# Optimization experiments

Measured on AMD Instinct MI355X. Metric: run time of the kernel, lower is better.

Reference implementation:

```python
import jax, jax.numpy as jnp
import numpy as np

B, N, NFEAT, NHID, NHEADS, NBLK = 8, 512, 32, 128, 4, 6


def _lrelu(x):
    return jax.nn.leaky_relu(x, 0.01)


def _layernorm(x, eps=1e-5):
    m = jnp.mean(x, axis=-1, keepdims=True)
    v = jnp.mean((x - m) ** 2, axis=-1, keepdims=True)
    return (x - m) / jnp.sqrt(v + eps)


def _gat(x, W, a, mask, concat):
    # x:[b,n,f]  W:[H,f,o]  a:[H,2o]  mask:[b,n,n] bool
    o = W.shape[-1]
    Wh = jnp.einsum('bnf,hfo->hbno', x, W)
    s1 = jnp.einsum('hbno,ho->hbn', Wh, a[:, :o])   # Wh @ a[:o]
    s2 = jnp.einsum('hbno,ho->hbn', Wh, a[:, o:])   # Wh @ a[o:]
    # rank-1 score: e[i,j] = leakyrelu(s1[i]*s2[j])
    e = _lrelu(s1[:, :, :, None] * s2[:, :, None, :])  # [h,b,n,n]
    e = jnp.where(mask[None], e, jnp.float32(-9e15))
    att = jax.nn.softmax(e, axis=-1)
    att = jnp.where(mask[None], att, jnp.float32(0.0))
    hp = jnp.einsum('hbij,hbjo->hbio', att, Wh)
    return jax.nn.elu(hp) if concat else hp


def _attn_block(x, W, a, rW, rb, mask):
    res = x
    h = _gat(x, W, a, mask, True)                      # [H,b,n,o]
    h = jnp.moveaxis(h, 0, 2).reshape(x.shape[0], x.shape[1], -1)  # concat heads
    h = h @ rW + rb
    if h.shape[-1] == res.shape[-1]:
        h = h + res
    return _layernorm(h)


def _fel(x, f1w1, f1b1, f1w2, f1b2, f2w1, f2b1, f2w2, f2b2, f3w1, f3b1, f3w2, f3b2):
    res = _lrelu(_lrelu(x @ f1w1 + f1b1) @ f1w2 + f1b2)
    h = _lrelu(_lrelu(res @ f2w1 + f2b1) @ f2w2 + f2b2)
    x = _layernorm(h + res)
    res = x
    h = _lrelu(res @ f3w1 + f3b1) @ f3w2 + f3b2
    return _layernorm(h + res)


def setup_inputs() -> dict:
    key = jax.random.key(0)
    ks = iter(jax.random.split(key, 24))
    nrm = lambda shape: jax.random.normal(next(ks), shape, jnp.float32) * 0.05
    inp = {}
    inp['x'] = jax.random.normal(next(ks), (B, N, NFEAT), jnp.float32)
    inp['adj'] = jax.random.randint(next(ks), (B, N, N), 0, 2, jnp.int32)
    inp['layer_id'] = 0
    inp['f1w1'] = nrm((NFEAT, NHID)); inp['f1b1'] = jnp.zeros((NHID,), jnp.float32)
    inp['f1w2'] = nrm((NHID, NHID)); inp['f1b2'] = jnp.zeros((NHID,), jnp.float32)
    inp['f2w1'] = nrm((NHID, 2 * NHID)); inp['f2b1'] = jnp.zeros((2 * NHID,), jnp.float32)
    inp['f2w2'] = nrm((2 * NHID, NHID)); inp['f2b2'] = jnp.zeros((NHID,), jnp.float32)
    inp['f3w1'] = nrm((NHID, 2 * NHID)); inp['f3b1'] = jnp.zeros((2 * NHID,), jnp.float32)
    inp['f3w2'] = nrm((2 * NHID, NHID)); inp['f3b2'] = jnp.zeros((NHID,), jnp.float32)
    inp['att_W'] = nrm((NBLK, NHEADS, NHID, NHID))
    inp['att_a'] = nrm((NBLK, NHEADS, 2 * NHID))
    inp['resh_W'] = nrm((NBLK, NHEADS * NHID, NHID))
    inp['resh_b'] = jnp.zeros((NBLK, NHID), jnp.float32)
    inp['out_W'] = nrm((2, NHID, NHID))
    inp['out_a'] = nrm((2, 2 * NHID))
    inp['proj_W'] = nrm((2 * NHID, 1))
    inp['proj_b'] = jnp.zeros((1,), jnp.float32)
    return inp


def reference(x, adj, layer_id, f1w1, f1b1, f1w2, f1b2, f2w1, f2b1, f2w2, f2b2,
              f3w1, f3b1, f3w2, f3b2, att_W, att_a, resh_W, resh_b, out_W, out_a,
              proj_W, proj_b):
    mask = adj > 0
    mask_t = jnp.transpose(adj, (0, 2, 1)) > 0
    h = _fel(x, f1w1, f1b1, f1w2, f1b2, f2w1, f2b1, f2w2, f2b2, f3w1, f3b1, f3w2, f3b2)
    for i in range(3):
        h = _attn_block(h, att_W[i], att_a[i], resh_W[i], resh_b[i], mask)
    h = _lrelu(_gat(h, out_W[0:1], out_a[0:1], mask, False)[0])
    ht = h
    for i in range(3, 6):
        ht = _attn_block(ht, att_W[i], att_a[i], resh_W[i], resh_b[i], mask_t)
    ht = _lrelu(_gat(ht, out_W[1:2], out_a[1:2], mask_t, False)[0])
    z = jnp.concatenate([h, ht], axis=-1)   # [b,n,2*nhid]
    z = jnp.mean(z, axis=1)                 # sum/length
    return jnp.squeeze(z @ proj_W + proj_b, axis=1)
```

## Files before the change

kernel.cpp:

```cpp
#include <hip/hip_runtime.h>
#include <math.h>

#define B 8
#define N 512
#define D 128
#define H 4
#define TOK (B*N)

typedef __attribute__((ext_vector_type(8))) short bfrag;
typedef __attribute__((ext_vector_type(4))) float facc;
typedef unsigned short u16;
typedef unsigned int u32;
typedef unsigned long long u64;

__device__ __forceinline__ float lrelu(float x){ return x > 0.f ? x : 0.01f*x; }
__device__ __forceinline__ u16 f2bf(float f){
  u32 u = __float_as_uint(f);
  u += 0x7fffu + ((u >> 16) & 1u);
  return (u16)(u >> 16);
}
__device__ __forceinline__ u32 pk2(float a, float b){
  return (u32)f2bf(a) | ((u32)f2bf(b) << 16);
}

#define LS 72

__global__ void prep_kernel(const int* __restrict__ adj,
    u32* __restrict__ mbits, u32* __restrict__ mtbits,
    const float* s0, const float* s1_, const float* s2_, const float* s3,
    const float* s4, const float* s5, const float* s6, const float* s7,
    const float* s8,
    u16* d0, u16* d1, u16* d2, u16* d3, u16* d4, u16* d5, u16* d6, u16* d7, u16* d8)
{
  __shared__ int smem[64*65];
  const int tid = threadIdx.x;
  if (blockIdx.x < 512){
    const int tb = blockIdx.x;
    const int b = tb >> 6, i0 = ((tb >> 3) & 7)*64, j0 = (tb & 7)*64;
    #pragma unroll
    for (int i = 0; i < 4; ++i){
      const int r = i*16 + (tid >> 4);
      const int c = (tid & 15)*4;
      int4 v = *(const int4*)&adj[((size_t)b*N + i0 + r)*N + j0 + c];
      smem[r*65 + c]     = v.x; smem[r*65 + c + 1] = v.y;
      smem[r*65 + c + 2] = v.z; smem[r*65 + c + 3] = v.w;
    }
    __syncthreads();
    const int wv = tid >> 6, lane = tid & 63;
    #pragma unroll
    for (int q = 0; q < 16; ++q){
      const int r = wv*16 + q;
      u64 bf_ = __ballot(smem[r*65 + lane] > 0);
      if (lane == 0)
        *(u64*)&mbits[((size_t)b*N + i0 + r)*16 + (j0 >> 5)] = bf_;
      u64 bt_ = __ballot(smem[lane*65 + r] > 0);
      if (lane == 0)
        *(u64*)&mtbits[((size_t)b*N + j0 + r)*16 + (i0 >> 5)] = bt_;
    }
  } else {
    float* ftile = (float*)smem;
    const int tx = tid & 31, ty = tid >> 5;
    const float* srcs[9] = {s0,s1_,s2_,s3,s4,s5,s6,s7,s8};
    u16* dsts[9] = {d0,d1,d2,d3,d4,d5,d6,d7,d8};
    const int Ks[9] = {32,128,128,256,128,256,128,128,512};
    const int Ns[9] = {128,128,256,128,256,128,128,128,128};
    const int zs[9] = {1,1,1,1,1,1,24,2,6};
    const int job = (int)blockIdx.x - 512;
    int m = 0, base = 0;
    for (; m < 9; ++m){
      int cnt = (Ks[m]>>5)*(Ns[m]>>5)*zs[m];
      if (job < base + cnt) break;
      base += cnt;
    }
    const int rem = job - base;
    const int tn = Ns[m] >> 5;
    const int per = (Ks[m] >> 5)*tn;
    const int z = rem / per, t = rem % per;
    const int k0 = (t / tn)*32, n0 = (t % tn)*32;
    const float* src = srcs[m] + (size_t)z*Ks[m]*Ns[m];
    u16* dst = dsts[m] + (size_t)z*Ks[m]*Ns[m];
    for (int r = ty; r < 32; r += 8)
      ftile[r*33 + tx] = src[(size_t)(k0+r)*Ns[m] + n0 + tx];
    __syncthreads();
    for (int r = ty; r < 32; r += 8)
      dst[(size_t)(n0+r)*Ks[m] + k0 + tx] = f2bf(ftile[tx*33 + r]);
  }
}

__device__ __forceinline__ void stageB64(const u16* __restrict__ BTn, int ldb,
                                         int k0, u16* Bs, int tid){
  const int n = tid >> 1, part = tid & 1;
  const u16* wp = BTn + (size_t)n*ldb + k0 + part*32;
  uint4 w0 = *(const uint4*)wp,      w1 = *(const uint4*)(wp+8);
  uint4 w2 = *(const uint4*)(wp+16), w3 = *(const uint4*)(wp+24);
  *(uint4*)&Bs[n*LS + part*32]      = w0;
  *(uint4*)&Bs[n*LS + part*32 + 8]  = w1;
  *(uint4*)&Bs[n*LS + part*32 + 16] = w2;
  *(uint4*)&Bs[n*LS + part*32 + 24] = w3;
}
__device__ __forceinline__ void stageB32(const u16* __restrict__ BTn, int ldb,
                                         int k0, u16* Bs, int tid){
  const int n = tid >> 1, part = tid & 1;
  const u16* wp = BTn + (size_t)n*ldb + k0 + part*16;
  uint4 w0 = *(const uint4*)wp, w1 = *(const uint4*)(wp+8);
  *(uint4*)&Bs[n*LS + part*16]     = w0;
  *(uint4*)&Bs[n*LS + part*16 + 8] = w1;
}

__device__ __forceinline__ void mfma64(const u16* As, const u16* Bs,
                                       facc acc[4], int r0, int c0,
                                       int quad, int l15){
  #pragma unroll
  for (int kk = 0; kk < 2; ++kk){
    bfrag af = *(const bfrag*)&As[(r0 + l15)*LS + kk*32 + quad*8];
    #pragma unroll
    for (int g = 0; g < 4; ++g){
      bfrag bf = *(const bfrag*)&Bs[(c0 + g*16 + l15)*LS + kk*32 + quad*8];
      acc[g] = __builtin_amdgcn_mfma_f32_16x16x32_bf16(af, bf, acc[g], 0,0,0);
    }
  }
}
__device__ __forceinline__ void mfma32(const u16* As, const u16* Bs,
                                       facc acc[4], int r0, int c0,
                                       int quad, int l15){
  bfrag af = *(const bfrag*)&As[(r0 + l15)*LS + quad*8];
  #pragma unroll
  for (int g = 0; g < 4; ++g){
    bfrag bf = *(const bfrag*)&Bs[(c0 + g*16 + l15)*LS + quad*8];
    acc[g] = __builtin_amdgcn_mfma_f32_16x16x32_bf16(af, bf, acc[g], 0,0,0);
  }
}

__device__ __forceinline__ void mfma64w(const u16* As, const u16* Bs,
                                        facc acc[2][2], int c0,
                                        int quad, int l15){
  #pragma unroll
  for (int kk = 0; kk < 2; ++kk){
    bfrag af0 = *(const bfrag*)&As[(l15)*LS      + kk*32 + quad*8];
    bfrag af1 = *(const bfrag*)&As[(16 + l15)*LS + kk*32 + quad*8];
    #pragma unroll
    for (int f = 0; f < 2; ++f){
      bfrag bf = *(const bfrag*)&Bs[(c0 + f*16 + l15)*LS + kk*32 + quad*8];
      acc[0][f] = __builtin_amdgcn_mfma_f32_16x16x32_bf16(af0, bf, acc[0][f], 0,0,0);
      acc[1][f] = __builtin_amdgcn_mfma_f32_16x16x32_bf16(af1, bf, acc[1][f], 0,0,0);
    }
  }
}

template<int ACT, int FIN>
__global__ __launch_bounds__(256) void gemm32(
    const float* __restrict__ A, int lda, int K,
    const u16* __restrict__ BT, const float* __restrict__ bias,
    const float* __restrict__ res, float* __restrict__ out, int ldo)
{
  const int tid = threadIdx.x;
  const int t0 = blockIdx.x * 32;
  const int n0 = blockIdx.y * 128;
  __shared__ __align__(16) u16 As[2][32*LS];
  __shared__ __align__(16) u16 Bs[2][128*LS];
  __shared__ float scrS[4][16], scrQ[4][16];
  const int wave = tid >> 6, lane = tid & 63, quad = lane >> 4, l15 = lane & 15;
  const int r0 = (wave & 1)*16, c0 = (wave >> 1)*64;
  facc acc[4];
  #pragma unroll
  for (int g = 0; g < 4; ++g) acc[g] = (facc){0.f,0.f,0.f,0.f};
  const u16* BTn = BT + (size_t)n0*K;

  const int arow = tid >> 3, ako = tid & 7;
  const float* aptr = A + (size_t)(t0+arow)*lda;
  const int bn = tid >> 1, bpart = tid & 1;
  const u16* bptr = BTn + (size_t)bn*K;

  const int nt = K >> 6;
  int kfin = 0;
  if (nt > 0){
    { const float* ap = aptr + ako*8;
      float4 a0 = *(const float4*)ap, a1 = *(const float4*)(ap+4);
      uint4 u = { pk2(a0.x,a0.y), pk2(a0.z,a0.w), pk2(a1.x,a1.y), pk2(a1.z,a1.w) };
      *(uint4*)&As[0][arow*LS + ako*8] = u;
      const u16* wp = bptr + bpart*32;
      uint4 g0 = *(const uint4*)wp,      g1 = *(const uint4*)(wp+8);
      uint4 g2 = *(const uint4*)(wp+16), g3 = *(const uint4*)(wp+24);
      u16* bp = &Bs[0][bn*LS + bpart*32];
      *(uint4*)bp = g0; *(uint4*)(bp+8) = g1; *(uint4*)(bp+16) = g2; *(uint4*)(bp+24) = g3;
    }
    __syncthreads();
    for (int k = 0; k < nt - 1; ++k){
      const int cur = k & 1, nxt = cur ^ 1;
      const float* ap = aptr + (k+1)*64 + ako*8;
      float4 a0 = *(const float4*)ap, a1 = *(const float4*)(ap+4);
      const u16* wp = bptr + (k+1)*64 + bpart*32;
      uint4 n0v = *(const uint4*)wp,      n1v = *(const uint4*)(wp+8);
      uint4 n2v = *(const uint4*)(wp+16), n3v = *(const uint4*)(wp+24);
      mfma64(As[cur], Bs[cur], acc, r0, c0, quad, l15);
      { uint4 u = { pk2(a0.x,a0.y), pk2(a0.z,a0.w), pk2(a1.x,a1.y), pk2(a1.z,a1.w) };
        *(uint4*)&As[nxt][arow*LS + ako*8] = u;
        u16* bp = &Bs[nxt][bn*LS + bpart*32];
        *(uint4*)bp = n0v; *(uint4*)(bp+8) = n1v; *(uint4*)(bp+16) = n2v; *(uint4*)(bp+24) = n3v; }
      __syncthreads();
    }
    kfin = (nt-1) & 1;
    mfma64(As[kfin], Bs[kfin], acc, r0, c0, quad, l15);
  }
  if (K & 63){
    if (nt > 0) __syncthreads();
    const int k0 = nt*64;
    { float4 a0 = *(const float4*)(aptr + k0 + ako*4);
      uint2 u = { pk2(a0.x,a0.y), pk2(a0.z,a0.w) };
      *(uint2*)&As[kfin][arow*LS + ako*4] = u;
    }
    stageB32(BTn, K, k0, Bs[kfin], tid);
    __syncthreads();
    mfma32(As[kfin], Bs[kfin], acc, r0, c0, quad, l15);
  }

  float bv[4];
  #pragma unroll
  for (int g = 0; g < 4; ++g) bv[g] = bias[n0 + c0 + g*16 + l15];

  if (FIN == 0){
    #pragma unroll
    for (int g = 0; g < 4; ++g){
      const int c = n0 + c0 + g*16 + l15;
      #pragma unroll
      for (int q = 0; q < 4; ++q){
        const int rq = t0 + r0 + quad*4 + q;
        float xv = acc[g][q] + bv[g];
        if (ACT) xv = lrelu(xv);
        out[(size_t)rq*ldo + c] = xv;
      }
    }
  } else {
    float v[4][4], s[4] = {0,0,0,0}, sq[4] = {0,0,0,0};
    #pragma unroll
    for (int g = 0; g < 4; ++g){
      const int c = c0 + g*16 + l15;
      #pragma unroll
      for (int q = 0; q < 4; ++q){
        const int rq = t0 + r0 + quad*4 + q;
        float xv = acc[g][q] + bv[g];
        if (ACT) xv = lrelu(xv);
        xv += res[(size_t)rq*128 + c];
        v[g][q] = xv; s[q] += xv; sq[q] += xv*xv;
      }
    }
    #pragma unroll
    for (int m = 1; m < 16; m <<= 1){
      #pragma unroll
      for (int q = 0; q < 4; ++q){ s[q] += __shfl_xor(s[q], m, 64); sq[q] += __shfl_xor(sq[q], m, 64); }
    }
    __syncthreads();
    if (l15 == 0){
      #pragma unroll
      for (int q = 0; q < 4; ++q){ scrS[wave][quad*4+q] = s[q]; scrQ[wave][quad*4+q] = sq[q]; }
    }
    __syncthreads();
    #pragma unroll
    for (int q = 0; q < 4; ++q){
      const int rq = t0 + r0 + quad*4 + q;
      const float fs = s[q] + scrS[wave^2][quad*4+q];
      const float fq = sq[q] + scrQ[wave^2][quad*4+q];
      const float mean = fs*(1.f/D);
      const float rstd = rsqrtf(fq*(1.f/D) - mean*mean + 1e-5f);
      #pragma unroll
      for (int g = 0; g < 4; ++g)
        out[(size_t)rq*128 + c0 + g*16 + l15] = (v[g][q] - mean)*rstd;
    }
  }
}

__global__ __launch_bounds__(256) void gemm32b(
    const u16* __restrict__ A, int lda, int K,
    const u16* __restrict__ BT, const float* __restrict__ bias,
    const float* __restrict__ res, float* __restrict__ out)
{
  const int tid = threadIdx.x;
  const int t0 = blockIdx.x * 32;
  __shared__ __align__(16) u16 As[2][32*LS];
  __shared__ __align__(16) u16 Bs[2][128*LS];
  __shared__ float scrS[4][32], scrQ[4][32];
  const int wave = tid >> 6, lane = tid & 63, quad = lane >> 4, l15 = lane & 15;
  const int c0 = wave*32;
  facc acc[2][2];
  #pragma unroll
  for (int rg = 0; rg < 2; ++rg)
    #pragma unroll
    for (int f = 0; f < 2; ++f) acc[rg][f] = (facc){0.f,0.f,0.f,0.f};

  const int arow = tid >> 3, ako = tid & 7;
  const u16* aptr = A + (size_t)(t0+arow)*lda + ako*8;
  const int bn = tid >> 1, bpart = tid & 1;
  const u16* bptr = BT + (size_t)bn*K + bpart*32;

  { uint4 ga = *(const uint4*)aptr;
    uint4 g0 = *(const uint4*)bptr,      g1 = *(const uint4*)(bptr+8);
    uint4 g2 = *(const uint4*)(bptr+16), g3 = *(const uint4*)(bptr+24);
    *(uint4*)&As[0][arow*LS + ako*8] = ga;
    u16* bp = &Bs[0][bn*LS + bpart*32];
    *(uint4*)bp = g0; *(uint4*)(bp+8) = g1; *(uint4*)(bp+16) = g2; *(uint4*)(bp+24) = g3;
  }
  __syncthreads();

  const int nt = K >> 6;
  for (int k = 0; k < nt - 1; ++k){
    const int cur = k & 1, nxt = cur ^ 1;
    uint4 na = *(const uint4*)(aptr + (k+1)*64);
    const u16* wp = bptr + (k+1)*64;
    uint4 n0 = *(const uint4*)wp,      n1 = *(const uint4*)(wp+8);
    uint4 n2 = *(const uint4*)(wp+16), n3 = *(const uint4*)(wp+24);
    mfma64w(As[cur], Bs[cur], acc, c0, quad, l15);
    *(uint4*)&As[nxt][arow*LS + ako*8] = na;
    { u16* bp = &Bs[nxt][bn*LS + bpart*32];
      *(uint4*)bp = n0; *(uint4*)(bp+8) = n1; *(uint4*)(bp+16) = n2; *(uint4*)(bp+24) = n3; }
    __syncthreads();
  }
  mfma64w(As[(nt-1)&1], Bs[(nt-1)&1], acc, c0, quad, l15);

  float bv[2];
  #pragma unroll
  for (int f = 0; f < 2; ++f) bv[f] = bias[c0 + f*16 + l15];
  float v[2][2][4], s[2][4], sq[2][4];
  #pragma unroll
  for (int rg = 0; rg < 2; ++rg)
    #pragma unroll
    for (int q = 0; q < 4; ++q){ s[rg][q] = 0.f; sq[rg][q] = 0.f; }
  #pragma unroll
  for (int rg = 0; rg < 2; ++rg){
    #pragma unroll
    for (int f = 0; f < 2; ++f){
      const int c = c0 + f*16 + l15;
      #pragma unroll
      for (int q = 0; q < 4; ++q){
        const int rq = t0 + rg*16 + quad*4 + q;
        float xv = acc[rg][f][q] + bv[f] + res[(size_t)rq*128 + c];
        v[rg][f][q] = xv; s[rg][q] += xv; sq[rg][q] += xv*xv;
      }
    }
  }
  #pragma unroll
  for (int m = 1; m < 16; m <<= 1){
    #pragma unroll
    for (int rg = 0; rg < 2; ++rg)
      #pragma unroll
      for (int q = 0; q < 4; ++q){ s[rg][q] += __shfl_xor(s[rg][q], m, 64); sq[rg][q] += __shfl_xor(sq[rg][q], m, 64); }
  }
  if (l15 == 0){
    #pragma unroll
    for (int rg = 0; rg < 2; ++rg)
      #pragma unroll
      for (int q = 0; q < 4; ++q){
        scrS[wave][rg*16 + quad*4 + q] = s[rg][q];
        scrQ[wave][rg*16 + quad*4 + q] = sq[rg][q];
      }
  }
  __syncthreads();
  #pragma unroll
  for (int rg = 0; rg < 2; ++rg){
    #pragma unroll
    for (int q = 0; q < 4; ++q){
      const int row = rg*16 + quad*4 + q;
      const float fs = scrS[0][row] + scrS[1][row] + scrS[2][row] + scrS[3][row];
      const float fq = scrQ[0][row] + scrQ[1][row] + scrQ[2][row] + scrQ[3][row];
      const float mean = fs*(1.f/D);
      const float rstd = rsqrtf(fq*(1.f/D) - mean*mean + 1e-5f);
      #pragma unroll
      for (int f = 0; f < 2; ++f)
        out[(size_t)(t0+row)*128 + c0 + f*16 + l15] = (v[rg][f][q] - mean)*rstd;
    }
  }
}

__global__ __launch_bounds__(256) void wh32(
    const float* __restrict__ hin, const u16* __restrict__ WT,
    const float* __restrict__ a, u16* __restrict__ WhT,
    float* __restrict__ s1, float* __restrict__ s2)
{
  const int tid = threadIdx.x;
  const int h  = blockIdx.x >> 7;
  const int t0 = (blockIdx.x & 127) * 32;
  const int b = t0 >> 9, j0 = t0 & (N-1);
  __shared__ __align__(16) u16 As[2][32*LS];
  __shared__ __align__(16) u16 Bs[2][128*LS];
  __shared__ float r1s[2][32], r2s[2][32];
  const int wave = tid >> 6, lane = tid & 63, quad = lane >> 4, l15 = lane & 15;
  const int r0 = (wave & 1)*16, c0 = (wave >> 1)*64;
  facc acc[4];
  #pragma unroll
  for (int g = 0; g < 4; ++g) acc[g] = (facc){0.f,0.f,0.f,0.f};

  const int arow = tid >> 3, ako = tid & 7;
  const float* aptr = hin + (size_t)(t0+arow)*D + ako*8;
  const int bn = tid >> 1, bpart = tid & 1;
  const u16* bwp = WT + (size_t)h*D*D + (size_t)bn*D + bpart*32;

  { float4 a0 = *(const float4*)aptr, a1 = *(const float4*)(aptr+4);
    uint4 u = { pk2(a0.x,a0.y), pk2(a0.z,a0.w), pk2(a1.x,a1.y), pk2(a1.z,a1.w) };
    *(uint4*)&As[0][arow*LS + ako*8] = u;
    uint4 g0 = *(const uint4*)bwp,      g1 = *(const uint4*)(bwp+8);
    uint4 g2 = *(const uint4*)(bwp+16), g3 = *(const uint4*)(bwp+24);
    u16* bp = &Bs[0][bn*LS + bpart*32];
    *(uint4*)bp = g0; *(uint4*)(bp+8) = g1; *(uint4*)(bp+16) = g2; *(uint4*)(bp+24) = g3;
  }
  __syncthreads();
  { float4 a0 = *(const float4*)(aptr+64), a1 = *(const float4*)(aptr+68);
    uint4 g0 = *(const uint4*)(bwp+64),    g1 = *(const uint4*)(bwp+72);
    uint4 g2 = *(const uint4*)(bwp+80),    g3 = *(const uint4*)(bwp+88);
    mfma64(As[0], Bs[0], acc, r0, c0, quad, l15);
    uint4 u = { pk2(a0.x,a0.y), pk2(a0.z,a0.w), pk2(a1.x,a1.y), pk2(a1.z,a1.w) };
    *(uint4*)&As[1][arow*LS + ako*8] = u;
    u16* bp = &Bs[1][bn*LS + bpart*32];
    *(uint4*)bp = g0; *(uint4*)(bp+8) = g1; *(uint4*)(bp+16) = g2; *(uint4*)(bp+24) = g3;
  }
  __syncthreads();
  mfma64(As[1], Bs[1], acc, r0, c0, quad, l15);

  const float* ah = a + (size_t)h*2*D;
  const size_t obase = (size_t)(h*8 + b)*128;
  float p1[4] = {0,0,0,0}, p2[4] = {0,0,0,0};
  #pragma unroll
  for (int g = 0; g < 4; ++g){
    const int c = c0 + g*16 + l15;
    const float a1v = ah[c], a2v = ah[D + c];
    ushort4 wv;
    wv.x = f2bf(acc[g][0]); wv.y = f2bf(acc[g][1]);
    wv.z = f2bf(acc[g][2]); wv.w = f2bf(acc[g][3]);
    *(ushort4*)&WhT[(obase + c)*N + j0 + r0 + quad*4] = wv;
    #pragma unroll
    for (int q = 0; q < 4; ++q){
      p1[q] = fmaf(acc[g][q], a1v, p1[q]);
      p2[q] = fmaf(acc[g][q], a2v, p2[q]);
    }
  }
  #pragma unroll
  for (int m = 1; m < 16; m <<= 1){
    #pragma unroll
    for (int q = 0; q < 4; ++q){ p1[q] += __shfl_xor(p1[q], m, 64); p2[q] += __shfl_xor(p2[q], m, 64); }
  }
  if (l15 == 0){
    #pragma unroll
    for (int q = 0; q < 4; ++q){
      r1s[wave>>1][r0 + quad*4 + q] = p1[q];
      r2s[wave>>1][r0 + quad*4 + q] = p2[q];
    }
  }
  __syncthreads();
  if (tid < 32){
    s1[(size_t)h*TOK + t0 + tid] = r1s[0][tid] + r1s[1][tid];
    s2[(size_t)h*TOK + t0 + tid] = r2s[0][tid] + r2s[1][tid];
  }
}

__device__ __forceinline__ float score8(const float* s2s, const unsigned char* mrow,
                                        float s1lr, int k0, int lq, u16* asp){
  float4 sa = *(const float4*)&s2s[k0 + lq*8];
  float4 sb = *(const float4*)&s2s[k0 + lq*8 + 4];
  const u32 mm = mrow[(k0 >> 3) + lq];
  float ss[8] = {sa.x,sa.y,sa.z,sa.w,sb.x,sb.y,sb.z,sb.w};
  float v[8]; float p = 0.f;
  #pragma unroll
  for (int i = 0; i < 8; ++i){
    float e = lrelu(s1lr * ss[i]);
    float ex = ((mm >> i) & 1u) ? __expf(e) : 0.f;
    v[i] = ex; p += ex;
  }
  uint4 u = { pk2(v[0],v[1]), pk2(v[2],v[3]), pk2(v[4],v[5]), pk2(v[6],v[7]) };
  *(uint4*)asp = u;
  return p;
}

template<int MODE, int OBF>
__global__ __launch_bounds__(256) void pv32(
    const float* __restrict__ s1, const float* __restrict__ s2,
    const u32* __restrict__ mbits, const u16* __restrict__ WhT,
    void* __restrict__ out_, int ldo, int hcs)
{
  const int tid = threadIdx.x;
  const int h  = blockIdx.x >> 7;
  const int t0 = (blockIdx.x & 127) * 32;
  const int b = t0 >> 9, i0 = t0 & (N-1);
  __shared__ float s2s[N];
  __shared__ float s1s[32], sums[32];
  __shared__ u32 mbs[32*16];
  __shared__ __align__(16) u16 As[2][32*LS];
  __shared__ __align__(16) u16 Bs[2][128*LS];

  s2s[tid]     = s2[(size_t)h*TOK + b*N + tid];
  s2s[tid+256] = s2[(size_t)h*TOK + b*N + tid + 256];
  if (tid < 32) s1s[tid] = s1[(size_t)h*TOK + t0 + tid];
  { const int r = tid >> 3, wd = (tid & 7)*2;
    *(uint2*)&mbs[r*16 + wd] = *(const uint2*)&mbits[((size_t)b*N + i0 + r)*16 + wd];
  }

  const u16* BTn = WhT + (size_t)(h*8 + b)*128*N;
  const int wave = tid >> 6, lane = tid & 63, quad = lane >> 4, l15 = lane & 15;
  const int c0 = wave*32;
  facc acc[2][2];
  #pragma unroll
  for (int rg = 0; rg < 2; ++rg)
    #pragma unroll
    for (int f = 0; f < 2; ++f) acc[rg][f] = (facc){0.f,0.f,0.f,0.f};

  const int lr = tid >> 3, lq = tid & 7;
  const unsigned char* mrow = (const unsigned char*)&mbs[lr*16];
  const int bn = tid >> 1, bpart = tid & 1;
  const u16* bwp = BTn + (size_t)bn*N + bpart*32;
  float psum = 0.f;

  uint4 g0 = *(const uint4*)bwp,      g1 = *(const uint4*)(bwp+8);
  uint4 g2 = *(const uint4*)(bwp+16), g3 = *(const uint4*)(bwp+24);
  __syncthreads();
  const float s1lr = s1s[lr];
  psum += score8(s2s, mrow, s1lr, 0, lq, &As[0][lr*LS + lq*8]);
  { u16* bp = &Bs[0][bn*LS + bpart*32];
    *(uint4*)bp = g0; *(uint4*)(bp+8) = g1; *(uint4*)(bp+16) = g2; *(uint4*)(bp+24) = g3; }
  __syncthreads();

  #pragma unroll
  for (int k = 0; k < 7; ++k){
    const int cur = k & 1, nxt = cur ^ 1;
    const u16* wp = bwp + (k+1)*64;
    uint4 n0 = *(const uint4*)wp,      n1 = *(const uint4*)(wp+8);
    uint4 n2 = *(const uint4*)(wp+16), n3 = *(const uint4*)(wp+24);
    psum += score8(s2s, mrow, s1lr, (k+1)*64, lq, &As[nxt][lr*LS + lq*8]);
    mfma64w(As[cur], Bs[cur], acc, c0, quad, l15);
    { u16* bp = &Bs[nxt][bn*LS + bpart*32];
      *(uint4*)bp = n0; *(uint4*)(bp+8) = n1; *(uint4*)(bp+16) = n2; *(uint4*)(bp+24) = n3; }
    __syncthreads();
  }
  mfma64w(As[1], Bs[1], acc, c0, quad, l15);

  #pragma unroll
  for (int m = 1; m < 8; m <<= 1) psum += __shfl_xor(psum, m, 64);
  if (lq == 0) sums[lr] = psum;
  __syncthreads();

  #pragma unroll
  for (int rg = 0; rg < 2; ++rg){
    #pragma unroll
    for (int q = 0; q < 4; ++q){
      const int row = rg*16 + quad*4 + q;
      const float sv = sums[row];
      const float inv = sv > 0.f ? 1.f/sv : 0.f;
      const int rq = t0 + row;
      #pragma unroll
      for (int f = 0; f < 2; ++f){
        float xv = acc[rg][f][q] * inv;
        xv = (MODE == 0) ? (xv > 0.f ? xv : __expf(xv) - 1.f) : lrelu(xv);
        const size_t idx = (size_t)rq*ldo + h*hcs + c0 + f*16 + l15;
        if (OBF) ((u16*)out_)[idx] = f2bf(xv);
        else     ((float*)out_)[idx] = xv;
      }
    }
  }
}

__global__ void final_kernel(const float* __restrict__ hF, const float* __restrict__ hT,
                             const float* __restrict__ pW, const float* __restrict__ pb,
                             float* __restrict__ out)
{
  const int b = blockIdx.x, c = threadIdx.x;
  __shared__ float scr[4];
  const float* src = (c < D) ? (hF + (size_t)b*N*D + c) : (hT + (size_t)b*N*D + (c - D));
  float s = 0.f;
  for (int n = 0; n < N; ++n) s += src[(size_t)n*D];
  s *= (1.f/N);
  float p = s * pW[c];
  #pragma unroll
  for (int m = 32; m; m >>= 1) p += __shfl_xor(p, m, 64);
  __syncthreads();
  if ((c & 63) == 0) scr[c >> 6] = p;
  __syncthreads();
  if (c == 0) out[b] = scr[0] + scr[1] + scr[2] + scr[3] + pb[0];
}

extern "C" void kernel_launch(void* const* d_in, const int* in_sizes, int n_in,
                              void* d_out, int out_size, void* d_ws, size_t ws_size,
                              hipStream_t stream)
{
  (void)in_sizes; (void)n_in; (void)out_size; (void)ws_size;
  const float* x    = (const float*)d_in[0];
  const int*   adj  = (const int*)d_in[1];
  const float* f1w1 = (const float*)d_in[3];
  const float* f1b1 = (const float*)d_in[4];
  const float* f1w2 = (const float*)d_in[5];
  const float* f1b2 = (const float*)d_in[6];
  const float* f2w1 = (const float*)d_in[7];
  const float* f2b1 = (const float*)d_in[8];
  const float* f2w2 = (const float*)d_in[9];
  const float* f2b2 = (const float*)d_in[10];
  const float* f3w1 = (const float*)d_in[11];
  const float* f3b1 = (const float*)d_in[12];
  const float* f3w2 = (const float*)d_in[13];
  const float* f3b2 = (const float*)d_in[14];
  const float* attW = (const float*)d_in[15];
  const float* attA = (const float*)d_in[16];
  const float* rshW = (const float*)d_in[17];
  const float* rshB = (const float*)d_in[18];
  const float* outW = (const float*)d_in[19];
  const float* outA = (const float*)d_in[20];
  const float* pW   = (const float*)d_in[21];
  const float* pb   = (const float*)d_in[22];

  char* w = (char*)d_ws;
  float* hA  = (float*)w; w += (size_t)TOK*128*4;
  float* hB  = (float*)w; w += (size_t)TOK*128*4;
  float* hF  = (float*)w; w += (size_t)TOK*128*4;
  float* hq  = (float*)w; w += (size_t)TOK*256*4;
  u16*  hp2  = (u16*)w;  w += (size_t)TOK*512*2;
  u16*  WhT  = (u16*)w;  w += (size_t)H*8*128*N*2;
  float* s1  = (float*)w; w += (size_t)H*TOK*4;
  float* s2  = (float*)w; w += (size_t)H*TOK*4;
  u32* mbits = (u32*)w;  w += (size_t)B*N*16*4;
  u32* mtbits= (u32*)w;  w += (size_t)B*N*16*4;
  u16* f1w1T = (u16*)w; w += 128*32*2;
  u16* f1w2T = (u16*)w; w += 128*128*2;
  u16* f2w1T = (u16*)w; w += 256*128*2;
  u16* f2w2T = (u16*)w; w += 128*256*2;
  u16* f3w1T = (u16*)w; w += 256*128*2;
  u16* f3w2T = (u16*)w; w += 128*256*2;
  u16* attWT = (u16*)w; w += (size_t)24*128*128*2;
  u16* outWT = (u16*)w; w += (size_t)2*128*128*2;
  u16* rshWT = (u16*)w; w += (size_t)6*128*512*2;

  prep_kernel<<<1460,256,0,stream>>>(adj, mbits, mtbits,
      f1w1, f1w2, f2w1, f2w2, f3w1, f3w2, attW, outW, rshW,
      f1w1T, f1w2T, f2w1T, f2w2T, f3w1T, f3w2T, attWT, outWT, rshWT);

  gemm32<1,0><<<dim3(128,1),256,0,stream>>>(x,   32, 32,  f1w1T, f1b1, nullptr, hF, 128);
  gemm32<1,0><<<dim3(128,1),256,0,stream>>>(hF, 128, 128, f1w2T, f1b2, nullptr, hB, 128);
  gemm32<1,0><<<dim3(128,2),256,0,stream>>>(hB, 128, 128, f2w1T, f2b1, nullptr, hq, 256);
  gemm32<1,1><<<dim3(128,1),256,0,stream>>>(hq, 256, 256, f2w2T, f2b2, hB, hF, 128);
  gemm32<1,0><<<dim3(128,2),256,0,stream>>>(hF, 128, 128, f3w1T, f3b1, nullptr, hq, 256);
  gemm32<0,1><<<dim3(128,1),256,0,stream>>>(hq, 256, 256, f3w2T, f3b2, hF, hA, 128);

  float* cur = hA; float* nxt = hB;
  for (int i = 0; i < 3; ++i){
    wh32<<<H*128,256,0,stream>>>(cur, attWT + (size_t)i*H*D*D,
                                 attA + (size_t)i*H*2*D, WhT, s1, s2);
    pv32<0,1><<<H*128,256,0,stream>>>(s1, s2, mbits, WhT, hp2, 512, 128);
    gemm32b<<<128,256,0,stream>>>(hp2, 512, 512,
        rshWT + (size_t)i*128*512, rshB + (size_t)i*D, cur, nxt);
    float* t_ = cur; cur = nxt; nxt = t_;
  }
  wh32<<<128,256,0,stream>>>(cur, outWT, outA, WhT, s1, s2);
  pv32<1,0><<<128,256,0,stream>>>(s1, s2, mbits, WhT, hF, 128, 0);

  cur = hF; nxt = hA;
  for (int i = 3; i < 6; ++i){
    wh32<<<H*128,256,0,stream>>>(cur, attWT + (size_t)i*H*D*D,
                                 attA + (size_t)i*H*2*D, WhT, s1, s2);
    pv32<0,1><<<H*128,256,0,stream>>>(s1, s2, mtbits, WhT, hp2, 512, 128);
    gemm32b<<<128,256,0,stream>>>(hp2, 512, 512,
        rshWT + (size_t)i*128*512, rshB + (size_t)i*D, cur, nxt);
    cur = nxt; nxt = (cur == hA) ? hB : hA;
  }
  wh32<<<128,256,0,stream>>>(cur, outWT + 128*128, outA + 2*D, WhT, s1, s2);
  pv32<1,0><<<128,256,0,stream>>>(s1, s2, mtbits, WhT, nxt, 128, 0);

  final_kernel<<<B,2*D,0,stream>>>(hF, nxt, pW, pb, (float*)d_out);
}
```

Baseline: 333.9 us.

## Fuse FEL MLP chain, reshape+Wh projection, and output GAT with next-block projection

Replaces the six separate FEL GEMM launches with one kernel that keeps every intermediate in shared memory as bf16 and then computes the first attention block's Wh projection and scores. The reshape GEMM is fused with the next block's Wh/score projection, and the output GAT kernel also computes the transposed branch's first projection, accumulating column sums with atomics so the final mean no longer rereads full activations. This cuts the launch count from about 27 to 16 and removes global round trips for intermediates. In exchange it adds register and shared-memory pressure, and fewer blocks (128) now carry the Wh work that previously ran on 512.

```diff
diff --git a/kernel.cpp b/kernel.cpp
--- a/kernel.cpp
+++ b/kernel.cpp
@@ -24,9 +24,12 @@
 }
 
 #define LS 72
+#define ASF 264
+#define ASW 136
 
 __global__ void prep_kernel(const int* __restrict__ adj,
     u32* __restrict__ mbits, u32* __restrict__ mtbits,
+    float* __restrict__ colsumF, float* __restrict__ colsumT,
     const float* s0, const float* s1_, const float* s2_, const float* s3,
     const float* s4, const float* s5, const float* s6, const float* s7,
     const float* s8,
@@ -57,7 +60,7 @@
       if (lane == 0)
         *(u64*)&mtbits[((size_t)b*N + j0 + r)*16 + (i0 >> 5)] = bt_;
     }
-  } else {
+  } else if (blockIdx.x < 1460){
     float* ftile = (float*)smem;
     const int tx = tid & 31, ty = tid >> 5;
     const float* srcs[9] = {s0,s1_,s2_,s3,s4,s5,s6,s7,s8};
@@ -84,19 +87,26 @@
     __syncthreads();
     for (int r = ty; r < 32; r += 8)
       dst[(size_t)(n0+r)*Ks[m] + k0 + tx] = f2bf(ftile[tx*33 + r]);
-  }
-}
-
-__device__ __forceinline__ void stageB64(const u16* __restrict__ BTn, int ldb,
-                                         int k0, u16* Bs, int tid){
+  } else {
+    float4 z = {0.f,0.f,0.f,0.f};
+    *(float4*)&colsumF[tid*4] = z;
+    *(float4*)&colsumT[tid*4] = z;
+  }
+}
+
+struct BPre { uint4 a,b,c,d; };
+__device__ __forceinline__ BPre preB64(const u16* __restrict__ BTn, int ldb, int k0, int tid){
   const int n = tid >> 1, part = tid & 1;
   const u16* wp = BTn + (size_t)n*ldb + k0 + part*32;
-  uint4 w0 = *(const uint4*)wp,      w1 = *(const uint4*)(wp+8);
-  uint4 w2 = *(const uint4*)(wp+16), w3 = *(const uint4*)(wp+24);
-  *(uint4*)&Bs[n*LS + part*32]      = w0;
-  *(uint4*)&Bs[n*LS + part*32 + 8]  = w1;
-  *(uint4*)&Bs[n*LS + part*32 + 16] = w2;
-  *(uint4*)&Bs[n*LS + part*32 + 24] = w3;
+  BPre r;
+  r.a = *(const uint4*)wp;      r.b = *(const uint4*)(wp+8);
+  r.c = *(const uint4*)(wp+16); r.d = *(const uint4*)(wp+24);
+  return r;
+}
+__device__ __forceinline__ void landB64(const BPre& p, u16* Bs, int tid){
+  const int n = tid >> 1, part = tid & 1;
+  u16* bp = &Bs[n*LS + part*32];
+  *(uint4*)bp = p.a; *(uint4*)(bp+8) = p.b; *(uint4*)(bp+16) = p.c; *(uint4*)(bp+24) = p.d;
 }
 __device__ __forceinline__ void stageB32(const u16* __restrict__ BTn, int ldb,
                                          int k0, u16* Bs, int tid){
@@ -107,12 +117,11 @@
   *(uint4*)&Bs[n*LS + part*16 + 8] = w1;
 }
 
-__device__ __forceinline__ void mfma64(const u16* As, const u16* Bs,
-                                       facc acc[4], int r0, int c0,
-                                       int quad, int l15){
+__device__ __forceinline__ void mfma64s(const u16* As, int sA, const u16* Bs,
+                                        facc acc[4], int r0, int c0, int quad, int l15){
   #pragma unroll
   for (int kk = 0; kk < 2; ++kk){
-    bfrag af = *(const bfrag*)&As[(r0 + l15)*LS + kk*32 + quad*8];
+    bfrag af = *(const bfrag*)&As[(r0 + l15)*sA + kk*32 + quad*8];
     #pragma unroll
     for (int g = 0; g < 4; ++g){
       bfrag bf = *(const bfrag*)&Bs[(c0 + g*16 + l15)*LS + kk*32 + quad*8];
@@ -120,17 +129,15 @@
     }
   }
 }
-__device__ __forceinline__ void mfma32(const u16* As, const u16* Bs,
-                                       facc acc[4], int r0, int c0,
-                                       int quad, int l15){
-  bfrag af = *(const bfrag*)&As[(r0 + l15)*LS + quad*8];
+__device__ __forceinline__ void mfma32s(const u16* As, int sA, const u16* Bs,
+                                        facc acc[4], int r0, int c0, int quad, int l15){
+  bfrag af = *(const bfrag*)&As[(r0 + l15)*sA + quad*8];
   #pragma unroll
   for (int g = 0; g < 4; ++g){
     bfrag bf = *(const bfrag*)&Bs[(c0 + g*16 + l15)*LS + quad*8];
     acc[g] = __builtin_amdgcn_mfma_f32_16x16x32_bf16(af, bf, acc[g], 0,0,0);
   }
 }
-
 __device__ __forceinline__ void mfma64w(const u16* As, const u16* Bs,
                                         facc acc[2][2], int c0,
                                         int quad, int l15){
@@ -147,100 +154,169 @@
   }
 }
 
-template<int ACT, int FIN>
-__global__ __launch_bounds__(256) void gemm32(
-    const float* __restrict__ A, int lda, int K,
-    const u16* __restrict__ BT, const float* __restrict__ bias,
-    const float* __restrict__ res, float* __restrict__ out, int ldo)
+template<int T>
+__device__ __forceinline__ void gemmAs(const u16* Aw, int sA,
+    const u16* __restrict__ BT, int ldb, u16* Bs,
+    facc acc[4], int tid, int r0, int c0, int quad, int l15){
+  BPre p = preB64(BT, ldb, 0, tid);
+  #pragma unroll
+  for (int t = 0; t < T; ++t){
+    __syncthreads();
+    landB64(p, Bs, tid);
+    if (t + 1 < T) p = preB64(BT, ldb, (t+1)*64, tid);
+    __syncthreads();
+    mfma64s(Aw + t*64, sA, Bs, acc, r0, c0, quad, l15);
+  }
+}
+
+template<int NH>
+__device__ __forceinline__ void wh_phaseS(const u16* Aw, int sA, u16* Bs,
+    const u16* __restrict__ WT, const float* __restrict__ aatt,
+    int t0, u16* __restrict__ WhT, float* __restrict__ s1, float* __restrict__ s2,
+    float (*r1s4)[2][32], float (*r2s4)[2][32], int tid)
+{
+  const int wave = tid >> 6, lane = tid & 63, quad = lane >> 4, l15 = lane & 15;
+  const int r0 = (wave & 1)*16, c0 = (wave >> 1)*64;
+  const int b = t0 >> 9, j0 = t0 & (N-1);
+  BPre p = preB64(WT, D, 0, tid);
+  facc acc[4];
+  #pragma unroll
+  for (int t = 0; t < 2*NH; ++t){
+    if ((t & 1) == 0){
+      #pragma unroll
+      for (int g = 0; g < 4; ++g) acc[g] = (facc){0.f,0.f,0.f,0.f};
+    }
+    __syncthreads();
+    landB64(p, Bs, tid);
+    if (t + 1 < 2*NH) p = preB64(WT + (size_t)((t+1)>>1)*D*D, D, ((t+1)&1)*64, tid);
+    __syncthreads();
+    mfma64s(Aw + (t&1)*64, sA, Bs, acc, r0, c0, quad, l15);
+    if (t & 1){
+      const int h = t >> 1;
+      const float* ah = aatt + (size_t)h*2*D;
+      const size_t obase = (size_t)(h*8 + b)*128;
+      float p1[4] = {0,0,0,0}, p2[4] = {0,0,0,0};
+      #pragma unroll
+      for (int g = 0; g < 4; ++g){
+        const int c = c0 + g*16 + l15;
+        const float a1v = ah[c], a2v = ah[D + c];
+        ushort4 wv;
+        wv.x = f2bf(acc[g][0]); wv.y = f2bf(acc[g][1]);
+        wv.z = f2bf(acc[g][2]); wv.w = f2bf(acc[g][3]);
+        *(ushort4*)&WhT[(obase + c)*N + j0 + r0 + quad*4] = wv;
+        #pragma unroll
+        for (int q = 0; q < 4; ++q){
+          p1[q] = fmaf(acc[g][q], a1v, p1[q]);
+          p2[q] = fmaf(acc[g][q], a2v, p2[q]);
+        }
+      }
+      #pragma unroll
+      for (int m = 1; m < 16; m <<= 1){
+        #pragma unroll
+        for (int q = 0; q < 4; ++q){ p1[q] += __shfl_xor(p1[q], m, 64); p2[q] += __shfl_xor(p2[q], m, 64); }
+      }
+      if (l15 == 0){
+        #pragma unroll
+        for (int q = 0; q < 4; ++q){
+          r1s4[h][wave>>1][r0 + quad*4 + q] = p1[q];
+          r2s4[h][wave>>1][r0 + quad*4 + q] = p2[q];
+        }
+      }
+    }
+  }
+  __syncthreads();
+  if (tid < 32*NH){
+    const int h = tid >> 5, r = tid & 31;
+    s1[(size_t)h*TOK + t0 + r] = r1s4[h][0][r] + r1s4[h][1][r];
+    s2[(size_t)h*TOK + t0 + r] = r2s4[h][0][r] + r2s4[h][1][r];
+  }
+}
+
+__global__ __launch_bounds__(256) void fel_kernel(
+    const float* __restrict__ x,
+    const u16* __restrict__ w1T, const float* __restrict__ b1,
+    const u16* __restrict__ w2T, const float* __restrict__ b2,
+    const u16* __restrict__ w3T, const float* __restrict__ b3,
+    const u16* __restrict__ w4T, const float* __restrict__ b4,
+    const u16* __restrict__ w5T, const float* __restrict__ b5,
+    const u16* __restrict__ w6T, const float* __restrict__ b6,
+    const u16* __restrict__ WTatt, const float* __restrict__ aatt,
+    float* __restrict__ hout, u16* __restrict__ WhT,
+    float* __restrict__ s1, float* __restrict__ s2)
 {
   const int tid = threadIdx.x;
   const int t0 = blockIdx.x * 32;
-  const int n0 = blockIdx.y * 128;
-  __shared__ __align__(16) u16 As[2][32*LS];
-  __shared__ __align__(16) u16 Bs[2][128*LS];
+  __shared__ __align__(16) u16 AwA[32*ASF];
+  __shared__ __align__(16) u16 AwB[32*ASF];
+  __shared__ __align__(16) u16 Bs[128*LS];
   __shared__ float scrS[4][16], scrQ[4][16];
+  __shared__ float r1s4[H][2][32], r2s4[H][2][32];
   const int wave = tid >> 6, lane = tid & 63, quad = lane >> 4, l15 = lane & 15;
   const int r0 = (wave & 1)*16, c0 = (wave >> 1)*64;
   facc acc[4];
+  float rres[4][4];
+
+  { const int row = tid >> 3, ko = tid & 7;
+    float4 a0 = *(const float4*)(x + (size_t)(t0+row)*32 + ko*4);
+    uint2 u = { pk2(a0.x,a0.y), pk2(a0.z,a0.w) };
+    *(uint2*)&AwA[row*ASF + ko*4] = u;
+    stageB32(w1T, 32, 0, Bs, tid);
+  }
+  __syncthreads();
   #pragma unroll
   for (int g = 0; g < 4; ++g) acc[g] = (facc){0.f,0.f,0.f,0.f};
-  const u16* BTn = BT + (size_t)n0*K;
-
-  const int arow = tid >> 3, ako = tid & 7;
-  const float* aptr = A + (size_t)(t0+arow)*lda;
-  const int bn = tid >> 1, bpart = tid & 1;
-  const u16* bptr = BTn + (size_t)bn*K;
-
-  const int nt = K >> 6;
-  int kfin = 0;
-  if (nt > 0){
-    { const float* ap = aptr + ako*8;
-      float4 a0 = *(const float4*)ap, a1 = *(const float4*)(ap+4);
-      uint4 u = { pk2(a0.x,a0.y), pk2(a0.z,a0.w), pk2(a1.x,a1.y), pk2(a1.z,a1.w) };
-      *(uint4*)&As[0][arow*LS + ako*8] = u;
-      const u16* wp = bptr + bpart*32;
-      uint4 g0 = *(const uint4*)wp,      g1 = *(const uint4*)(wp+8);
-      uint4 g2 = *(const uint4*)(wp+16), g3 = *(const uint4*)(wp+24);
-      u16* bp = &Bs[0][bn*LS + bpart*32];
-      *(uint4*)bp = g0; *(uint4*)(bp+8) = g1; *(uint4*)(bp+16) = g2; *(uint4*)(bp+24) = g3;
-    }
-    __syncthreads();
-    for (int k = 0; k < nt - 1; ++k){
-      const int cur = k & 1, nxt = cur ^ 1;
-      const float* ap = aptr + (k+1)*64 + ako*8;
-      float4 a0 = *(const float4*)ap, a1 = *(const float4*)(ap+4);
-      const u16* wp = bptr + (k+1)*64 + bpart*32;
-      uint4 n0v = *(const uint4*)wp,      n1v = *(const uint4*)(wp+8);
-      uint4 n2v = *(const uint4*)(wp+16), n3v = *(const uint4*)(wp+24);
-      mfma64(As[cur], Bs[cur], acc, r0, c0, quad, l15);
-      { uint4 u = { pk2(a0.x,a0.y), pk2(a0.z,a0.w), pk2(a1.x,a1.y), pk2(a1.z,a1.w) };
-        *(uint4*)&As[nxt][arow*LS + ako*8] = u;
-        u16* bp = &Bs[nxt][bn*LS + bpart*32];
-        *(uint4*)bp = n0v; *(uint4*)(bp+8) = n1v; *(uint4*)(bp+16) = n2v; *(uint4*)(bp+24) = n3v; }
-      __syncthreads();
-    }
-    kfin = (nt-1) & 1;
-    mfma64(As[kfin], Bs[kfin], acc, r0, c0, quad, l15);
-  }
-  if (K & 63){
-    if (nt > 0) __syncthreads();
-    const int k0 = nt*64;
-    { float4 a0 = *(const float4*)(aptr + k0 + ako*4);
-      uint2 u = { pk2(a0.x,a0.y), pk2(a0.z,a0.w) };
-      *(uint2*)&As[kfin][arow*LS + ako*4] = u;
-    }
-    stageB32(BTn, K, k0, Bs[kfin], tid);
-    __syncthreads();
-    mfma32(As[kfin], Bs[kfin], acc, r0, c0, quad, l15);
-  }
-
-  float bv[4];
-  #pragma unroll
-  for (int g = 0; g < 4; ++g) bv[g] = bias[n0 + c0 + g*16 + l15];
-
-  if (FIN == 0){
-    #pragma unroll
-    for (int g = 0; g < 4; ++g){
-      const int c = n0 + c0 + g*16 + l15;
-      #pragma unroll
-      for (int q = 0; q < 4; ++q){
-        const int rq = t0 + r0 + quad*4 + q;
-        float xv = acc[g][q] + bv[g];
-        if (ACT) xv = lrelu(xv);
-        out[(size_t)rq*ldo + c] = xv;
-      }
-    }
-  } else {
-    float v[4][4], s[4] = {0,0,0,0}, sq[4] = {0,0,0,0};
+  mfma32s(AwA, ASF, Bs, acc, r0, c0, quad, l15);
+  #pragma unroll
+  for (int g = 0; g < 4; ++g){
+    const int c = c0 + g*16 + l15;
+    const float bv = b1[c];
+    #pragma unroll
+    for (int q = 0; q < 4; ++q)
+      AwB[(r0 + quad*4 + q)*ASF + c] = f2bf(lrelu(acc[g][q] + bv));
+  }
+
+  #pragma unroll
+  for (int g = 0; g < 4; ++g) acc[g] = (facc){0.f,0.f,0.f,0.f};
+  gemmAs<2>(AwB, ASF, w2T, 128, Bs, acc, tid, r0, c0, quad, l15);
+  #pragma unroll
+  for (int g = 0; g < 4; ++g){
+    const int c = c0 + g*16 + l15;
+    const float bv = b2[c];
+    #pragma unroll
+    for (int q = 0; q < 4; ++q){
+      float xv = lrelu(acc[g][q] + bv);
+      AwA[(r0 + quad*4 + q)*ASF + c] = f2bf(xv);
+      rres[g][q] = xv;
+    }
+  }
+
+  #pragma unroll
+  for (int ch = 0; ch < 2; ++ch){
+    #pragma unroll
+    for (int g = 0; g < 4; ++g) acc[g] = (facc){0.f,0.f,0.f,0.f};
+    gemmAs<2>(AwA, ASF, w3T + (size_t)ch*128*128, 128, Bs, acc, tid, r0, c0, quad, l15);
     #pragma unroll
     for (int g = 0; g < 4; ++g){
       const int c = c0 + g*16 + l15;
+      const float bv = b3[ch*128 + c];
+      #pragma unroll
+      for (int q = 0; q < 4; ++q)
+        AwB[(r0 + quad*4 + q)*ASF + ch*128 + c] = f2bf(lrelu(acc[g][q] + bv));
+    }
+  }
+
+  #pragma unroll
+  for (int g = 0; g < 4; ++g) acc[g] = (facc){0.f,0.f,0.f,0.f};
+  gemmAs<4>(AwB, ASF, w4T, 256, Bs, acc, tid, r0, c0, quad, l15);
+  {
+    float v[4][4], s[4] = {0,0,0,0}, sq[4] = {0,0,0,0};
+    #pragma unroll
+    for (int g = 0; g < 4; ++g){
+      const int c = c0 + g*16 + l15;
+      const float bv = b4[c];
       #pragma unroll
       for (int q = 0; q < 4; ++q){
-        const int rq = t0 + r0 + quad*4 + q;
-        float xv = acc[g][q] + bv[g];
-        if (ACT) xv = lrelu(xv);
-        xv += res[(size_t)rq*128 + c];
+        float xv = lrelu(acc[g][q] + bv) + rres[g][q];
         v[g][q] = xv; s[q] += xv; sq[q] += xv*xv;
       }
     }
@@ -249,7 +325,6 @@
       #pragma unroll
       for (int q = 0; q < 4; ++q){ s[q] += __shfl_xor(s[q], m, 64); sq[q] += __shfl_xor(sq[q], m, 64); }
     }
-    __syncthreads();
     if (l15 == 0){
       #pragma unroll
       for (int q = 0; q < 4; ++q){ scrS[wave][quad*4+q] = s[q]; scrQ[wave][quad*4+q] = sq[q]; }
@@ -257,30 +332,95 @@
     __syncthreads();
     #pragma unroll
     for (int q = 0; q < 4; ++q){
-      const int rq = t0 + r0 + quad*4 + q;
+      const int r = r0 + quad*4 + q;
       const float fs = s[q] + scrS[wave^2][quad*4+q];
       const float fq = sq[q] + scrQ[wave^2][quad*4+q];
       const float mean = fs*(1.f/D);
       const float rstd = rsqrtf(fq*(1.f/D) - mean*mean + 1e-5f);
       #pragma unroll
-      for (int g = 0; g < 4; ++g)
-        out[(size_t)rq*128 + c0 + g*16 + l15] = (v[g][q] - mean)*rstd;
-    }
-  }
-}
-
-__global__ __launch_bounds__(256) void gemm32b(
-    const u16* __restrict__ A, int lda, int K,
-    const u16* __restrict__ BT, const float* __restrict__ bias,
-    const float* __restrict__ res, float* __restrict__ out)
+      for (int g = 0; g < 4; ++g){
+        const int c = c0 + g*16 + l15;
+        float xv = (v[g][q] - mean)*rstd;
+        AwA[r*ASF + c] = f2bf(xv);
+        rres[g][q] = xv;
+      }
+    }
+  }
+
+  #pragma unroll
+  for (int ch = 0; ch < 2; ++ch){
+    #pragma unroll
+    for (int g = 0; g < 4; ++g) acc[g] = (facc){0.f,0.f,0.f,0.f};
+    gemmAs<2>(AwA, ASF, w5T + (size_t)ch*128*128, 128, Bs, acc, tid, r0, c0, quad, l15);
+    #pragma unroll
+    for (int g = 0; g < 4; ++g){
+      const int c = c0 + g*16 + l15;
+      const float bv = b5[ch*128 + c];
+      #pragma unroll
+      for (int q = 0; q < 4; ++q)
+        AwB[(r0 + quad*4 + q)*ASF + ch*128 + c] = f2bf(lrelu(acc[g][q] + bv));
+    }
+  }
+
+  #pragma unroll
+  for (int g = 0; g < 4; ++g) acc[g] = (facc){0.f,0.f,0.f,0.f};
+  gemmAs<4>(AwB, ASF, w6T, 256, Bs, acc, tid, r0, c0, quad, l15);
+  {
+    float v[4][4], s[4] = {0,0,0,0}, sq[4] = {0,0,0,0};
+    #pragma unroll
+    for (int g = 0; g < 4; ++g){
+      const int c = c0 + g*16 + l15;
+      const float bv = b6[c];
+      #pragma unroll
+      for (int q = 0; q < 4; ++q){
+        float xv = acc[g][q] + bv + rres[g][q];
+        v[g][q] = xv; s[q] += xv; sq[q] += xv*xv;
+      }
+    }
+    #pragma unroll
+    for (int m = 1; m < 16; m <<= 1){
+      #pragma unroll
+      for (int q = 0; q < 4; ++q){ s[q] += __shfl_xor(s[q], m, 64); sq[q] += __shfl_xor(sq[q], m, 64); }
+    }
+    if (l15 == 0){
+      #pragma unroll
+      for (int q = 0; q < 4; ++q){ scrS[wave][quad*4+q] = s[q]; scrQ[wave][quad*4+q] = sq[q]; }
+    }
+    __syncthreads();
+    #pragma unroll
+    for (int q = 0; q < 4; ++q){
+      const int r = r0 + quad*4 + q;
+      const float fs = s[q] + scrS[wave^2][quad*4+q];
+      const float fq = sq[q] + scrQ[wave^2][quad*4+q];
+      const float mean = fs*(1.f/D);
+      const float rstd = rsqrtf(fq*(1.f/D) - mean*mean + 1e-5f);
+      #pragma unroll
+      for (int g = 0; g < 4; ++g){
+        const int c = c0 + g*16 + l15;
+        float xv = (v[g][q] - mean)*rstd;
+        hout[(size_t)(t0 + r)*128 + c] = xv;
+        AwA[r*ASF + c] = f2bf(xv);
+      }
+    }
+  }
+  wh_phaseS<H>(AwA, ASF, Bs, WTatt, aatt, t0, WhT, s1, s2, r1s4, r2s4, tid);
+}
+
+template<int NH>
+__global__ __launch_bounds__(256) void reshwh(
+    const u16* __restrict__ A, const u16* __restrict__ BT, const float* __restrict__ bias,
+    const float* __restrict__ res, float* __restrict__ hout,
+    const u16* __restrict__ WT, const float* __restrict__ aatt,
+    u16* __restrict__ WhT, float* __restrict__ s1, float* __restrict__ s2)
 {
   const int tid = threadIdx.x;
   const int t0 = blockIdx.x * 32;
-  __shared__ __align__(16) u16 As[2][32*LS];
+  __shared__ __align__(16) u16 AsU[2][32*LS];
   __shared__ __align__(16) u16 Bs[2][128*LS];
   __shared__ float scrS[4][32], scrQ[4][32];
+  __shared__ float r1s4[NH][2][32], r2s4[NH][2][32];
   const int wave = tid >> 6, lane = tid & 63, quad = lane >> 4, l15 = lane & 15;
-  const int c0 = wave*32;
+  const int c0w = wave*32;
   facc acc[2][2];
   #pragma unroll
   for (int rg = 0; rg < 2; ++rg)
@@ -288,37 +428,36 @@
     for (int f = 0; f < 2; ++f) acc[rg][f] = (facc){0.f,0.f,0.f,0.f};
 
   const int arow = tid >> 3, ako = tid & 7;
-  const u16* aptr = A + (size_t)(t0+arow)*lda + ako*8;
+  const u16* aptr = A + (size_t)(t0+arow)*512 + ako*8;
   const int bn = tid >> 1, bpart = tid & 1;
-  const u16* bptr = BT + (size_t)bn*K + bpart*32;
+  const u16* bptr = BT + (size_t)bn*512 + bpart*32;
 
   { uint4 ga = *(const uint4*)aptr;
     uint4 g0 = *(const uint4*)bptr,      g1 = *(const uint4*)(bptr+8);
     uint4 g2 = *(const uint4*)(bptr+16), g3 = *(const uint4*)(bptr+24);
-    *(uint4*)&As[0][arow*LS + ako*8] = ga;
+    *(uint4*)&AsU[0][arow*LS + ako*8] = ga;
     u16* bp = &Bs[0][bn*LS + bpart*32];
     *(uint4*)bp = g0; *(uint4*)(bp+8) = g1; *(uint4*)(bp+16) = g2; *(uint4*)(bp+24) = g3;
   }
   __syncthreads();
-
-  const int nt = K >> 6;
-  for (int k = 0; k < nt - 1; ++k){
+  #pragma unroll
+  for (int k = 0; k < 7; ++k){
     const int cur = k & 1, nxt = cur ^ 1;
     uint4 na = *(const uint4*)(aptr + (k+1)*64);
     const u16* wp = bptr + (k+1)*64;
     uint4 n0 = *(const uint4*)wp,      n1 = *(const uint4*)(wp+8);
     uint4 n2 = *(const uint4*)(wp+16), n3 = *(const uint4*)(wp+24);
-    mfma64w(As[cur], Bs[cur], acc, c0, quad, l15);
-    *(uint4*)&As[nxt][arow*LS + ako*8] = na;
+    mfma64w(AsU[cur], Bs[cur], acc, c0w, quad, l15);
+    *(uint4*)&AsU[nxt][arow*LS + ako*8] = na;
     { u16* bp = &Bs[nxt][bn*LS + bpart*32];
       *(uint4*)bp = n0; *(uint4*)(bp+8) = n1; *(uint4*)(bp+16) = n2; *(uint4*)(bp+24) = n3; }
     __syncthreads();
   }
-  mfma64w(As[(nt-1)&1], Bs[(nt-1)&1], acc, c0, quad, l15);
+  mfma64w(AsU[1], Bs[1], acc, c0w, quad, l15);
 
   float bv[2];
   #pragma unroll
-  for (int f = 0; f < 2; ++f) bv[f] = bias[c0 + f*16 + l15];
+  for (int f = 0; f < 2; ++f) bv[f] = bias[c0w + f*16 + l15];
   float v[2][2][4], s[2][4], sq[2][4];
   #pragma unroll
   for (int rg = 0; rg < 2; ++rg)
@@ -328,7 +467,7 @@
   for (int rg = 0; rg < 2; ++rg){
     #pragma unroll
     for (int f = 0; f < 2; ++f){
-      const int c = c0 + f*16 + l15;
+      const int c = c0w + f*16 + l15;
       #pragma unroll
       for (int q = 0; q < 4; ++q){
         const int rq = t0 + rg*16 + quad*4 + q;
@@ -354,6 +493,7 @@
       }
   }
   __syncthreads();
+  u16* Aw = &AsU[0][0];
   #pragma unroll
   for (int rg = 0; rg < 2; ++rg){
     #pragma unroll
@@ -364,90 +504,15 @@
       const float mean = fs*(1.f/D);
       const float rstd = rsqrtf(fq*(1.f/D) - mean*mean + 1e-5f);
       #pragma unroll
-      for (int f = 0; f < 2; ++f)
-        out[(size_t)(t0+row)*128 + c0 + f*16 + l15] = (v[rg][f][q] - mean)*rstd;
-    }
-  }
-}
-
-__global__ __launch_bounds__(256) void wh32(
-    const float* __restrict__ hin, const u16* __restrict__ WT,
-    const float* __restrict__ a, u16* __restrict__ WhT,
-    float* __restrict__ s1, float* __restrict__ s2)
-{
-  const int tid = threadIdx.x;
-  const int h  = blockIdx.x >> 7;
-  const int t0 = (blockIdx.x & 127) * 32;
-  const int b = t0 >> 9, j0 = t0 & (N-1);
-  __shared__ __align__(16) u16 As[2][32*LS];
-  __shared__ __align__(16) u16 Bs[2][128*LS];
-  __shared__ float r1s[2][32], r2s[2][32];
-  const int wave = tid >> 6, lane = tid & 63, quad = lane >> 4, l15 = lane & 15;
-  const int r0 = (wave & 1)*16, c0 = (wave >> 1)*64;
-  facc acc[4];
-  #pragma unroll
-  for (int g = 0; g < 4; ++g) acc[g] = (facc){0.f,0.f,0.f,0.f};
-
-  const int arow = tid >> 3, ako = tid & 7;
-  const float* aptr = hin + (size_t)(t0+arow)*D + ako*8;
-  const int bn = tid >> 1, bpart = tid & 1;
-  const u16* bwp = WT + (size_t)h*D*D + (size_t)bn*D + bpart*32;
-
-  { float4 a0 = *(const float4*)aptr, a1 = *(const float4*)(aptr+4);
-    uint4 u = { pk2(a0.x,a0.y), pk2(a0.z,a0.w), pk2(a1.x,a1.y), pk2(a1.z,a1.w) };
-    *(uint4*)&As[0][arow*LS + ako*8] = u;
-    uint4 g0 = *(const uint4*)bwp,      g1 = *(const uint4*)(bwp+8);
-    uint4 g2 = *(const uint4*)(bwp+16), g3 = *(const uint4*)(bwp+24);
-    u16* bp = &Bs[0][bn*LS + bpart*32];
-    *(uint4*)bp = g0; *(uint4*)(bp+8) = g1; *(uint4*)(bp+16) = g2; *(uint4*)(bp+24) = g3;
-  }
-  __syncthreads();
-  { float4 a0 = *(const float4*)(aptr+64), a1 = *(const float4*)(aptr+68);
-    uint4 g0 = *(const uint4*)(bwp+64),    g1 = *(const uint4*)(bwp+72);
-    uint4 g2 = *(const uint4*)(bwp+80),    g3 = *(const uint4*)(bwp+88);
-    mfma64(As[0], Bs[0], acc, r0, c0, quad, l15);
-    uint4 u = { pk2(a0.x,a0.y), pk2(a0.z,a0.w), pk2(a1.x,a1.y), pk2(a1.z,a1.w) };
-    *(uint4*)&As[1][arow*LS + ako*8] = u;
-    u16* bp = &Bs[1][bn*LS + bpart*32];
-    *(uint4*)bp = g0; *(uint4*)(bp+8) = g1; *(uint4*)(bp+16) = g2; *(uint4*)(bp+24) = g3;
-  }
-  __syncthreads();
-  mfma64(As[1], Bs[1], acc, r0, c0, quad, l15);
-
-  const float* ah = a + (size_t)h*2*D;
-  const size_t obase = (size_t)(h*8 + b)*128;
-  float p1[4] = {0,0,0,0}, p2[4] = {0,0,0,0};
-  #pragma unroll
-  for (int g = 0; g < 4; ++g){
-    const int c = c0 + g*16 + l15;
-    const float a1v = ah[c], a2v = ah[D + c];
-    ushort4 wv;
-    wv.x = f2bf(acc[g][0]); wv.y = f2bf(acc[g][1]);
-    wv.z = f2bf(acc[g][2]); wv.w = f2bf(acc[g][3]);
-    *(ushort4*)&WhT[(obase + c)*N + j0 + r0 + quad*4] = wv;
-    #pragma unroll
-    for (int q = 0; q < 4; ++q){
-      p1[q] = fmaf(acc[g][q], a1v, p1[q]);
-      p2[q] = fmaf(acc[g][q], a2v, p2[q]);
-    }
-  }
-  #pragma unroll
-  for (int m = 1; m < 16; m <<= 1){
-    #pragma unroll
-    for (int q = 0; q < 4; ++q){ p1[q] += __shfl_xor(p1[q], m, 64); p2[q] += __shfl_xor(p2[q], m, 64); }
-  }
-  if (l15 == 0){
-    #pragma unroll
-    for (int q = 0; q < 4; ++q){
-      r1s[wave>>1][r0 + quad*4 + q] = p1[q];
-      r2s[wave>>1][r0 + quad*4 + q] = p2[q];
-    }
-  }
-  __syncthreads();
-  if (tid < 32){
-    s1[(size_t)h*TOK + t0 + tid] = r1s[0][tid] + r1s[1][tid];
-    s2[(size_t)h*TOK + t0 + tid] = r2s[0][tid] + r2s[1][tid];
-  }
+      for (int f = 0; f < 2; ++f){
+        const int c = c0w + f*16 + l15;
+        float xv = (v[rg][f][q] - mean)*rstd;
+        hout[(size_t)(t0+row)*128 + c] = xv;
+        Aw[row*ASW + c] = f2bf(xv);
+      }
+    }
+  }
+  wh_phaseS<NH>(Aw, ASW, &Bs[0][0], WT, aatt, t0, WhT, s1, s2, r1s4, r2s4, tid);
 }
 
 __device__ __forceinline__ float score8(const float* s2s, const unsigned char* mrow,
@@ -468,11 +533,10 @@
   return p;
 }
 
-template<int MODE, int OBF>
 __global__ __launch_bounds__(256) void pv32(
     const float* __restrict__ s1, const float* __restrict__ s2,
     const u32* __restrict__ mbits, const u16* __restrict__ WhT,
-    void* __restrict__ out_, int ldo, int hcs)
+    u16* __restrict__ out_)
 {
   const int tid = threadIdx.x;
   const int h  = blockIdx.x >> 7;
@@ -545,29 +609,122 @@
       #pragma unroll
       for (int f = 0; f < 2; ++f){
         float xv = acc[rg][f][q] * inv;
-        xv = (MODE == 0) ? (xv > 0.f ? xv : __expf(xv) - 1.f) : lrelu(xv);
-        const size_t idx = (size_t)rq*ldo + h*hcs + c0 + f*16 + l15;
-        if (OBF) ((u16*)out_)[idx] = f2bf(xv);
-        else     ((float*)out_)[idx] = xv;
-      }
-    }
-  }
-}
-
-__global__ void final_kernel(const float* __restrict__ hF, const float* __restrict__ hT,
+        xv = xv > 0.f ? xv : __expf(xv) - 1.f;
+        out_[(size_t)rq*512 + h*128 + c0 + f*16 + l15] = f2bf(xv);
+      }
+    }
+  }
+}
+
+template<int DOWH>
+__global__ __launch_bounds__(256) void pvout(
+    const float* __restrict__ s1in, const float* __restrict__ s2in,
+    const u32* __restrict__ mbits, const u16* __restrict__ WhTin,
+    float* __restrict__ hF, float* __restrict__ colsum,
+    const u16* __restrict__ WT, const float* __restrict__ aatt,
+    u16* __restrict__ WhTout, float* __restrict__ s1out, float* __restrict__ s2out)
+{
+  const int tid = threadIdx.x;
+  const int t0 = blockIdx.x * 32;
+  const int b = t0 >> 9, i0 = t0 & (N-1);
+  __shared__ float s2s[N];
+  __shared__ float s1s[32], sums[32];
+  __shared__ u32 mbs[32*16];
+  __shared__ __align__(16) u16 AsU[2][32*LS];
+  __shared__ __align__(16) u16 Bs[2][128*LS];
+  __shared__ float r1s4[H][2][32], r2s4[H][2][32];
+
+  s2s[tid]     = s2in[b*N + tid];
+  s2s[tid+256] = s2in[b*N + tid + 256];
+  if (tid < 32) s1s[tid] = s1in[t0 + tid];
+  { const int r = tid >> 3, wd = (tid & 7)*2;
+    *(uint2*)&mbs[r*16 + wd] = *(const uint2*)&mbits[((size_t)b*N + i0 + r)*16 + wd];
+  }
+
+  const u16* BTn = WhTin + (size_t)b*128*N;
+  const int wave = tid >> 6, lane = tid & 63, quad = lane >> 4, l15 = lane & 15;
+  const int c0w = wave*32;
+  facc acc[2][2];
+  #pragma unroll
+  for (int rg = 0; rg < 2; ++rg)
+    #pragma unroll
+    for (int f = 0; f < 2; ++f) acc[rg][f] = (facc){0.f,0.f,0.f,0.f};
+
+  const int lr = tid >> 3, lq = tid & 7;
+  const unsigned char* mrow = (const unsigned char*)&mbs[lr*16];
+  const int bn = tid >> 1, bpart = tid & 1;
+  const u16* bwp = BTn + (size_t)bn*N + bpart*32;
+  float psum = 0.f;
+
+  uint4 g0 = *(const uint4*)bwp,      g1 = *(const uint4*)(bwp+8);
+  uint4 g2 = *(const uint4*)(bwp+16), g3 = *(const uint4*)(bwp+24);
+  __syncthreads();
+  const float s1lr = s1s[lr];
+  psum += score8(s2s, mrow, s1lr, 0, lq, &AsU[0][lr*LS + lq*8]);
+  { u16* bp = &Bs[0][bn*LS + bpart*32];
+    *(uint4*)bp = g0; *(uint4*)(bp+8) = g1; *(uint4*)(bp+16) = g2; *(uint4*)(bp+24) = g3; }
+  __syncthreads();
+
+  #pragma unroll
+  for (int k = 0; k < 7; ++k){
+    const int cur = k & 1, nxt = cur ^ 1;
+    const u16* wp = bwp + (k+1)*64;
+    uint4 n0 = *(const uint4*)wp,      n1 = *(const uint4*)(wp+8);
+    uint4 n2 = *(const uint4*)(wp+16), n3 = *(const uint4*)(wp+24);
+    psum += score8(s2s, mrow, s1lr, (k+1)*64, lq, &AsU[nxt][lr*LS + lq*8]);
+    mfma64w(AsU[cur], Bs[cur], acc, c0w, quad, l15);
+    { u16* bp = &Bs[nxt][bn*LS + bpart*32];
+      *(uint4*)bp = n0; *(uint4*)(bp+8) = n1; *(uint4*)(bp+16) = n2; *(uint4*)(bp+24) = n3; }
+    __syncthreads();
+  }
+  mfma64w(AsU[1], Bs[1], acc, c0w, quad, l15);
+
+  #pragma unroll
+  for (int m = 1; m < 8; m <<= 1) psum += __shfl_xor(psum, m, 64);
+  if (lq == 0) sums[lr] = psum;
+  __syncthreads();
+
+  u16* Aw = &AsU[0][0];
+  float pcs[2] = {0.f, 0.f};
+  #pragma unroll
+  for (int rg = 0; rg < 2; ++rg){
+    #pragma unroll
+    for (int q = 0; q < 4; ++q){
+      const int row = rg*16 + quad*4 + q;
+      const float sv = sums[row];
+      const float inv = sv > 0.f ? 1.f/sv : 0.f;
+      #pragma unroll
+      for (int f = 0; f < 2; ++f){
+        const int c = c0w + f*16 + l15;
+        float xv = lrelu(acc[rg][f][q] * inv);
+        if (DOWH){
+          hF[(size_t)(t0+row)*128 + c] = xv;
+          Aw[row*ASW + c] = f2bf(xv);
+        }
+        pcs[f] += xv;
+      }
+    }
+  }
+  pcs[0] += __shfl_xor(pcs[0], 16, 64); pcs[0] += __shfl_xor(pcs[0], 32, 64);
+  pcs[1] += __shfl_xor(pcs[1], 16, 64); pcs[1] += __shfl_xor(pcs[1], 32, 64);
+  if (quad == 0){
+    atomicAdd(&colsum[b*128 + c0w + l15], pcs[0]);
+    atomicAdd(&colsum[b*128 + c0w + 16 + l15], pcs[1]);
+  }
+  if (DOWH)
+    wh_phaseS<H>(Aw, ASW, &Bs[0][0], WT, aatt, t0, WhTout, s1out, s2out, r1s4, r2s4, tid);
+}
+
+__global__ void final_kernel(const float* __restrict__ colsumF, const float* __restrict__ colsumT,
                              const float* __restrict__ pW, const float* __restrict__ pb,
                              float* __restrict__ out)
 {
   const int b = blockIdx.x, c = threadIdx.x;
   __shared__ float scr[4];
-  const float* src = (c < D) ? (hF + (size_t)b*N*D + c) : (hT + (size_t)b*N*D + (c - D));
-  float s = 0.f;
-  for (int n = 0; n < N; ++n) s += src[(size_t)n*D];
-  s *= (1.f/N);
+  float s = ((c < D) ? colsumF[b*D + c] : colsumT[b*D + (c - D)]) * (1.f/N);
   float p = s * pW[c];
   #pragma unroll
   for (int m = 32; m; m >>= 1) p += __shfl_xor(p, m, 64);
-  __syncthreads();
   if ((c & 63) == 0) scr[c >> 6] = p;
   __syncthreads();
   if (c == 0) out[b] = scr[0] + scr[1] + scr[2] + scr[3] + pb[0];
@@ -605,13 +762,17 @@
   float* hA  = (float*)w; w += (size_t)TOK*128*4;
   float* hB  = (float*)w; w += (size_t)TOK*128*4;
   float* hF  = (float*)w; w += (size_t)TOK*128*4;
-  float* hq  = (float*)w; w += (size_t)TOK*256*4;
   u16*  hp2  = (u16*)w;  w += (size_t)TOK*512*2;
   u16*  WhT  = (u16*)w;  w += (size_t)H*8*128*N*2;
+  u16*  WhT2 = (u16*)w;  w += (size_t)H*8*128*N*2;
   float* s1  = (float*)w; w += (size_t)H*TOK*4;
   float* s2  = (float*)w; w += (size_t)H*TOK*4;
+  float* s1b = (float*)w; w += (size_t)H*TOK*4;
+  float* s2b = (float*)w; w += (size_t)H*TOK*4;
   u32* mbits = (u32*)w;  w += (size_t)B*N*16*4;
   u32* mtbits= (u32*)w;  w += (size_t)B*N*16*4;
+  float* colsumF = (float*)w; w += (size_t)B*128*4;
+  float* colsumT = (float*)w; w += (size_t)B*128*4;
   u16* f1w1T = (u16*)w; w += 128*32*2;
   u16* f1w2T = (u16*)w; w += 128*128*2;
   u16* f2w1T = (u16*)w; w += 256*128*2;
@@ -622,40 +783,39 @@
   u16* outWT = (u16*)w; w += (size_t)2*128*128*2;
   u16* rshWT = (u16*)w; w += (size_t)6*128*512*2;
 
-  prep_kernel<<<1460,256,0,stream>>>(adj, mbits, mtbits,
+  prep_kernel<<<1461,256,0,stream>>>(adj, mbits, mtbits, colsumF, colsumT,
       f1w1, f1w2, f2w1, f2w2, f3w1, f3w2, attW, outW, rshW,
       f1w1T, f1w2T, f2w1T, f2w2T, f3w1T, f3w2T, attWT, outWT, rshWT);
 
-  gemm32<1,0><<<dim3(128,1),256,0,stream>>>(x,   32, 32,  f1w1T, f1b1, nullptr, hF, 128);
-  gemm32<1,0><<<dim3(128,1),256,0,stream>>>(hF, 128, 128, f1w2T, f1b2, nullptr, hB, 128);
-  gemm32<1,0><<<dim3(128,2),256,0,stream>>>(hB, 128, 128, f2w1T, f2b1, nullptr, hq, 256);
-  gemm32<1,1><<<dim3(128,1),256,0,stream>>>(hq, 256, 256, f2w2T, f2b2, hB, hF, 128);
-  gemm32<1,0><<<dim3(128,2),256,0,stream>>>(hF, 128, 128, f3w1T, f3b1, nullptr, hq, 256);
-  gemm32<0,1><<<dim3(128,1),256,0,stream>>>(hq, 256, 256, f3w2T, f3b2, hF, hA, 128);
-
-  float* cur = hA; float* nxt = hB;
-  for (int i = 0; i < 3; ++i){
-    wh32<<<H*128,256,0,stream>>>(cur, attWT + (size_t)i*H*D*D,
-                                 attA + (size_t)i*H*2*D, WhT, s1, s2);
-    pv32<0,1><<<H*128,256,0,stream>>>(s1, s2, mbits, WhT, hp2, 512, 128);
-    gemm32b<<<128,256,0,stream>>>(hp2, 512, 512,
-        rshWT + (size_t)i*128*512, rshB + (size_t)i*D, cur, nxt);
-    float* t_ = cur; cur = nxt; nxt = t_;
-  }
-  wh32<<<128,256,0,stream>>>(cur, outWT, outA, WhT, s1, s2);
-  pv32<1,0><<<128,256,0,stream>>>(s1, s2, mbits, WhT, hF, 128, 0);
-
-  cur = hF; nxt = hA;
-  for (int i = 3; i < 6; ++i){
-    wh32<<<H*128,256,0,stream>>>(cur, attWT + (size_t)i*H*D*D,
-                                 attA + (size_t)i*H*2*D, WhT, s1, s2);
-    pv32<0,1><<<H*128,256,0,stream>>>(s1, s2, mtbits, WhT, hp2, 512, 128);
-    gemm32b<<<128,256,0,stream>>>(hp2, 512, 512,
-        rshWT + (size_t)i*128*512, rshB + (size_t)i*D, cur, nxt);
-    cur = nxt; nxt = (cur == hA) ? hB : hA;
-  }
-  wh32<<<128,256,0,stream>>>(cur, outWT + 128*128, outA + 2*D, WhT, s1, s2);
-  pv32<1,0><<<128,256,0,stream>>>(s1, s2, mtbits, WhT, nxt, 128, 0);
-
-  final_kernel<<<B,2*D,0,stream>>>(hF, nxt, pW, pb, (float*)d_out);
-}
+  fel_kernel<<<128,256,0,stream>>>(x,
+      f1w1T, f1b1, f1w2T, f1b2, f2w1T, f2b1, f2w2T, f2b2, f3w1T, f3b1, f3w2T, f3b2,
+      attWT, attA, hA, WhT, s1, s2);
+
+  pv32<<<H*128,256,0,stream>>>(s1, s2, mbits, WhT, hp2);
+  reshwh<4><<<128,256,0,stream>>>(hp2, rshWT + 0*128*512, rshB + 0*D, hA, hB,
+      attWT + (size_t)1*H*D*D, attA + (size_t)1*H*2*D, WhT, s1, s2);
+  pv32<<<H*128,256,0,stream>>>(s1, s2, mbits, WhT, hp2);
+  reshwh<4><<<128,256,0,stream>>>(hp2, rshWT + (size_t)1*128*512, rshB + 1*D, hB, hA,
+      attWT + (size_t)2*H*D*D, attA + (size_t)2*H*2*D, WhT, s1, s2);
+  pv32<<<H*128,256,0,stream>>>(s1, s2, mbits, WhT, hp2);
+  reshwh<1><<<128,256,0,stream>>>(hp2, rshWT + (size_t)2*128*512, rshB + 2*D, hA, hB,
+      outWT, outA, WhT, s1, s2);
+
+  pvout<1><<<128,256,0,stream>>>(s1, s2, mbits, WhT, hF, colsumF,
+      attWT + (size_t)3*H*D*D, attA + (size_t)3*H*2*D, WhT2, s1b, s2b);
+
+  pv32<<<H*128,256,0,stream>>>(s1b, s2b, mtbits, WhT2, hp2);
+  reshwh<4><<<128,256,0,stream>>>(hp2, rshWT + (size_t)3*128*512, rshB + 3*D, hF, hA,
+      attWT + (size_t)4*H*D*D, attA + (size_t)4*H*2*D, WhT, s1, s2);
+  pv32<<<H*128,256,0,stream>>>(s1, s2, mtbits, WhT, hp2);
+  reshwh<4><<<128,256,0,stream>>>(hp2, rshWT + (size_t)4*128*512, rshB + 4*D, hA, hB,
+      attWT + (size_t)5*H*D*D, attA + (size_t)5*H*2*D, WhT, s1, s2);
+  pv32<<<H*128,256,0,stream>>>(s1, s2, mtbits, WhT, hp2);
+  reshwh<1><<<128,256,0,stream>>>(hp2, rshWT + (size_t)5*128*512, rshB + 5*D, hB, hA,
+      outWT + 128*128, outA + 2*D, WhT, s1, s2);
+
+  pvout<0><<<128,256,0,stream>>>(s1, s2, mtbits, WhT, nullptr, colsumT,
+      nullptr, nullptr, nullptr, nullptr, nullptr);
+
+  final_kernel<<<B,2*D,0,stream>>>(colsumF, colsumT, pW, pb, (float*)d_out);
+}
```

Measured after the change: 307.5 us. 1.09x faster.
